# Performance work log

Hardware: AMD Instinct MI355X
Metric: run time of the kernel (lower is better)

Reference implementation:

```python
import jax, jax.numpy as jnp
import numpy as np

B, C, T, L, H = 1024, 32, 9, 24, 8
D = C // H
TOKEN_LEN = 24

def _l2norm(x, eps=1e-12):
    n = jnp.linalg.norm(x, axis=-1, keepdims=True)
    return x / jnp.maximum(n, eps)

def setup_inputs() -> dict:
    key = jax.random.key(0)
    ks = jax.random.split(key, 16)
    def lin_w(k, din, dout):
        return (jax.random.uniform(k, (din, dout), jnp.float32) - 0.5) * (2.0 / np.sqrt(din))
    def lin_b(k, dout, din):
        return (jax.random.uniform(k, (dout,), jnp.float32) - 0.5) * (2.0 / np.sqrt(din))
    inp = {}
    inp['x'] = jax.random.normal(ks[0], (B, C, T, L), jnp.float32)
    inp['Wq'] = lin_w(ks[1], C, C); inp['bq'] = lin_b(ks[2], C, C)
    inp['Wk'] = lin_w(ks[3], C, C); inp['bk'] = lin_b(ks[4], C, C)
    inp['Wv'] = lin_w(ks[5], C, C); inp['bv'] = lin_b(ks[6], C, C)
    inp['Wm'] = lin_w(ks[7], C, C); inp['bm'] = lin_b(ks[8], C, C)
    inp['W_logit'] = jnp.eye(H, dtype=jnp.float32)
    inp['W_ctx'] = jnp.eye(H, dtype=jnp.float32)
    inp['rel_pos_bias'] = jax.random.normal(ks[9], (H, 2 * TOKEN_LEN - 1), jnp.float32) * 0.02
    inp['pre_prompt'] = jax.random.normal(ks[10], (1, C, T, TOKEN_LEN), jnp.float32) * 0.02
    inp['conv_w'] = jax.random.normal(ks[11], (C, C, 3, 3), jnp.float32) / np.sqrt(C * 9)
    inp['conv_b'] = jnp.zeros((C,), jnp.float32)
    inp['bn_gamma'] = jnp.ones((C,), jnp.float32)
    inp['bn_beta'] = jnp.zeros((C,), jnp.float32)
    inp['bn_mean'] = jax.random.normal(ks[12], (C,), jnp.float32) * 0.1
    inp['bn_var'] = jax.random.uniform(ks[13], (C,), jnp.float32) * 0.5 + 0.75
    inp['p_w'] = lin_w(ks[14], TOKEN_LEN, 6).T  # torch Linear(24,6) weight: (6,24)
    inp['p_b'] = lin_b(ks[15], 6, TOKEN_LEN)
    inp['atten_flag'] = 2
    return inp

def reference(x, Wq, bq, Wk, bk, Wv, bv, Wm, bm, W_logit, W_ctx, rel_pos_bias,
              pre_prompt, conv_w, conv_b, bn_gamma, bn_beta, bn_mean, bn_var,
              p_w, p_b, atten_flag):
    b, c, t, l = x.shape
    xp = jnp.transpose(x, (0, 2, 3, 1))  # (b,t,l,c)
    def heads(W, bias):
        y = xp @ W + bias
        return jnp.transpose(y.reshape(b, t, l, H, D), (0, 1, 3, 2, 4))  # (b,t,h,l,d)
    q = _l2norm(heads(Wq, bq))
    k = _l2norm(heads(Wk, bk))
    v = _l2norm(heads(Wv, bv))
    logits = jnp.einsum('bthid,bthjd->bthij', q, k) / np.sqrt(D).astype(np.float32)
    idx = jnp.arange(l)
    rel = jnp.clip(idx[:, None] - idx[None, :] + TOKEN_LEN - 1, 0, 2 * TOKEN_LEN - 2)
    logits = logits + rel_pos_bias[:, rel][None, None]  # bias: (h,l,l)
    logits = jnp.einsum('bthij,hH->btHij', logits, W_logit)
    attn = jax.nn.softmax(logits, axis=-1)
    attn = jnp.einsum('bthij,hH->btHij', attn, W_ctx)
    x_att = jnp.einsum('bthij,bthjd->bthid', attn, v)
    x_att = jnp.transpose(x_att, (0, 1, 3, 2, 4)).reshape(b, t, l, c) @ Wm + bm
    x_att = jnp.transpose(x_att, (0, 3, 1, 2))  # (b,c,t,l)
    pre = jnp.broadcast_to(pre_prompt, (b, c, t, l))
    if atten_flag == 1:
        con = jnp.concatenate([x_att[..., :18], pre[..., 18:]], -1); tar = x_att[..., 18:]
    elif atten_flag == 2:
        con = jnp.concatenate([x_att[..., :12], pre[..., 12:18], x_att[..., 18:]], -1); tar = x_att[..., 12:18]
    elif atten_flag == 3:
        con = jnp.concatenate([x_att[..., :6], pre[..., 6:12], x_att[..., 12:]], -1); tar = x_att[..., 6:12]
    else:
        con = jnp.concatenate([pre[..., :6], x_att[..., 6:]], -1); tar = x_att[..., :6]
    # ConvNormAct(32,32,3,1): Conv2d(3x3, same pad) + BatchNorm2d(eval) + ReLU
    y = jax.lax.conv_general_dilated(con, conv_w, (1, 1), 'SAME',
                                     dimension_numbers=('NCHW', 'OIHW', 'NCHW'))
    y = y + conv_b[None, :, None, None]
    y = (y - bn_mean[None, :, None, None]) * jax.lax.rsqrt(bn_var[None, :, None, None] + 1e-5)
    y = y * bn_gamma[None, :, None, None] + bn_beta[None, :, None, None]
    y = jax.nn.relu(y)
    p = jnp.einsum('bctl,ol->bcto', y, p_w) + p_b  # Linear(token_len, 6) on last dim
    p = tar - p
    if atten_flag == 1:
        out = jnp.concatenate([x_att[..., :18], p], -1)
    elif atten_flag == 2:
        out = jnp.concatenate([x_att[..., :12], p, x_att[..., 18:]], -1)
    elif atten_flag == 3:
        out = jnp.concatenate([x_att[..., :6], p, x_att[..., 12:]], -1)
    else:
        out = jnp.concatenate([p, x_att[..., 6:]], -1)
    return out  # dropout is identity in eval mode
```

## Files before the change

kernel.cpp:

```cpp
#include <hip/hip_runtime.h>
#include <hip/hip_bf16.h>

#define NB   1024
#define NC   32
#define NT   9
#define NL   24
#define CTL  6912
#define TOK  216
#define QSTR 872
#define NTHR 512

typedef _Float16 f16x8 __attribute__((ext_vector_type(8)));
typedef _Float16 f16x4 __attribute__((ext_vector_type(4)));
typedef float    f32x4 __attribute__((ext_vector_type(4)));

#define OFF_BIGA 0
#define SZ_BIGA  41856
#define OFF_BIGB (OFF_BIGA + SZ_BIGA)
#define OFF_WM   (OFF_BIGB + 7680)
#define OFF_BIGC (OFF_WM + 2560)
#define OFF_SPRE (OFF_BIGC + 20480)
#define OFF_REL  (OFF_SPRE + 4320)
#define OFF_WL   (OFF_REL + 1504)
#define OFF_WC   (OFF_WL + 256)
#define OFF_BQKV (OFF_WC + 256)
#define OFF_BM   (OFF_BQKV + 384)
#define OFF_AC   (OFF_BM + 128)
#define OFF_BC   (OFF_AC + 128)
#define OFF_PW   (OFF_BC + 128)
#define OFF_PB   (OFF_PW + 576)
#define OFF_FLG  (OFF_PB + 24)
#define POOL_SZ  80288

static __device__ __forceinline__ float ldf(const void* p, size_t i, bool f32) {
    return f32 ? ((const float*)p)[i]
               : __bfloat162float(((const __hip_bfloat16*)p)[i]);
}
static __device__ __forceinline__ void stf(void* p, size_t i, float v, bool f32) {
    if (f32) ((float*)p)[i] = v;
    else     ((__hip_bfloat16*)p)[i] = __float2bfloat16(v);
}
static __device__ __forceinline__ f32x4 mfma16(f16x8 a, f16x8 b, f32x4 c) {
    return __builtin_amdgcn_mfma_f32_16x16x32_f16(a, b, c, 0, 0, 0);
}

__global__ __launch_bounds__(NTHR, 4) void fused_kernel(
    const void* __restrict__ x,
    const void* __restrict__ Wq, const void* __restrict__ bq,
    const void* __restrict__ Wk, const void* __restrict__ bk,
    const void* __restrict__ Wv, const void* __restrict__ bv,
    const void* __restrict__ Wm, const void* __restrict__ bm,
    const void* __restrict__ Wl, const void* __restrict__ Wc,
    const void* __restrict__ rel, const void* __restrict__ pre,
    const void* __restrict__ cw, const void* __restrict__ cb,
    const void* __restrict__ gmm, const void* __restrict__ bta,
    const void* __restrict__ mean, const void* __restrict__ var,
    const void* __restrict__ p_w, const void* __restrict__ p_b,
    const int* __restrict__ atten_flag,
    void* __restrict__ out)
{
    __shared__ __align__(16) char pool[POOL_SZ];

    const bool f32p = (((const unsigned*)Wl)[0] == 0x3F800000u);
    const int tid  = threadIdx.x;
    const int b    = blockIdx.x;
    const int lane = tid & 63;
    const int wave = tid >> 6;
    const int l15  = lane & 15;
    const int quad = lane >> 4;
    const int grp  = lane & ~7;

    const int flag = atten_flag[0];
    const int s = (flag == 1) ? 18 : (flag == 2) ? 12 : (flag == 3) ? 6 : 0;

    {
        _Float16* xT  = (_Float16*)(pool + OFF_BIGA);
        _Float16* atH = (_Float16*)(pool + OFF_BIGC);
        _Float16* Wqk = (_Float16*)(pool + OFF_BIGB);
        _Float16* WmH = (_Float16*)(pool + OFF_WM);
        _Float16* prH = (_Float16*)(pool + OFF_SPRE);
        float* relF = (float*)(pool + OFF_REL);
        float* wlF  = (float*)(pool + OFF_WL);
        float* wcF  = (float*)(pool + OFF_WC);
        float* bqk  = (float*)(pool + OFF_BQKV);
        float* bmF  = (float*)(pool + OFF_BM);
        float* acF  = (float*)(pool + OFF_AC);
        float* bcF  = (float*)(pool + OFF_BC);
        float* pwF  = (float*)(pool + OFF_PW);
        float* pbF  = (float*)(pool + OFF_PB);

        for (int i = tid; i < CTL; i += NTHR) {
            int c = i / TOK, tok = i % TOK;
            xT[tok*40 + c] = (_Float16)ldf(x, (size_t)b*CTL + i, f32p);
        }
        for (int i = tid; i < 1600; i += NTHR) {
            xT[8640 + i]  = (_Float16)0.f;
            atH[8640 + i] = (_Float16)0.f;
        }
        for (int i = tid; i < 3072; i += NTHR) {
            int mat = i >> 10, r = i & 1023, ci = r >> 5, co = r & 31;
            const void* W = (mat == 0) ? Wq : (mat == 1) ? Wk : Wv;
            Wqk[(mat*32 + co)*40 + ci] = (_Float16)ldf(W, r, f32p);
        }
        for (int i = tid; i < 1024; i += NTHR) {
            int ci = i >> 5, co = i & 31;
            WmH[co*40 + ci] = (_Float16)ldf(Wm, i, f32p);
        }
        for (int i = tid; i < 1728; i += NTHR) {
            int ci = i / 54, r = i % 54, tt = r / 6, o = r % 6;
            prH[(tt*6 + o)*40 + ci] = (_Float16)ldf(pre, (ci*9 + tt)*24 + s + o, f32p);
        }
        for (int i = tid; i < 376; i += NTHR) relF[i] = ldf(rel, i, f32p);
        if (tid < 64)  wlF[tid] = ldf(Wl, tid, f32p);
        if (tid >= 64 && tid < 128) wcF[tid-64] = ldf(Wc, tid-64, f32p);
        if (tid >= 128 && tid < 224) {
            int i = tid - 128; int mat = i >> 5;
            const void* bb = (mat == 0) ? bq : (mat == 1) ? bk : bv;
            bqk[i] = ldf(bb, i & 31, f32p);
        }
        if (tid >= 224 && tid < 256) bmF[tid-224] = ldf(bm, tid-224, f32p);
        if (tid < 32) {
            float rs = rsqrtf(ldf(var, tid, f32p) + 1e-5f);
            float A  = ldf(gmm, tid, f32p) * rs;
            acF[tid] = A;
            bcF[tid] = (ldf(cb, tid, f32p) - ldf(mean, tid, f32p)) * A
                       + ldf(bta, tid, f32p);
        }
        if (tid >= 32 && tid < 176) pwF[tid-32] = ldf(p_w, tid-32, f32p);
        if (tid >= 176 && tid < 182) pbF[tid-176] = ldf(p_b, tid-176, f32p);
    }
    __syncthreads();

    if (tid < 2) {
        const float* M = (const float*)(pool + (tid == 0 ? OFF_WL : OFF_WC));
        int id = 1;
        for (int i = 0; i < 64; i++)
            id &= (M[i] == ((i % 9 == 0) ? 1.f : 0.f));
        ((int*)(pool + OFF_FLG))[tid] = id;
    }

    {
        const _Float16* xT  = (const _Float16*)(pool + OFF_BIGA);
        const _Float16* Wqk = (const _Float16*)(pool + OFF_BIGB);
        f32x4 acc[2][6];
        #pragma unroll
        for (int im = 0; im < 2; im++)
            #pragma unroll
            for (int nt = 0; nt < 6; nt++) acc[im][nt] = 0.f;
        f16x8 bfr[6];
        #pragma unroll
        for (int nt = 0; nt < 6; nt++)
            bfr[nt] = *(const f16x8*)(Wqk + (nt*16 + l15)*40 + quad*8);
        #pragma unroll
        for (int im = 0; im < 2; im++) {
            const int mt = wave + im*8;
            if (mt < 14) {
                f16x8 a = *(const f16x8*)(xT + (mt*16 + l15)*40 + quad*8);
                #pragma unroll
                for (int nt = 0; nt < 6; nt++)
                    acc[im][nt] = mfma16(a, bfr[nt], acc[im][nt]);
            }
        }
        __syncthreads();
        _Float16* qH = (_Float16*)(pool + OFF_BIGA);
        const float* bqk = (const float*)(pool + OFF_BQKV);
        #pragma unroll
        for (int im = 0; im < 2; im++) {
            const int mt = wave + im*8;
            if (mt < 14) {
                #pragma unroll
                for (int nt = 0; nt < 6; nt++) {
                    int co = nt*16 + l15;
                    int mat = co >> 5, hc = co & 31;
                    _Float16* dst = qH + (mat*8 + (hc >> 2))*QSTR + (hc & 3);
                    float bias = bqk[co];
                    #pragma unroll
                    for (int r = 0; r < 4; r++) {
                        int tok = mt*16 + quad*4 + r;
                        if (tok < 216) dst[tok*4] = (_Float16)(acc[im][nt][r] + bias);
                    }
                }
            }
        }
    }
    __syncthreads();

    {
        _Float16* qH = (_Float16*)(pool + OFF_BIGA);
        for (int idx = tid; idx < 3*8*216; idx += NTHR) {
            int plane = idx / 216, tok = idx % 216;
            f16x4* pv = (f16x4*)(qH + plane*QSTR + tok*4);
            f16x4 v = *pv;
            float a0 = v[0], a1 = v[1], a2 = v[2], a3 = v[3];
            float s2 = a0*a0 + a1*a1 + a2*a2 + a3*a3;
            float sc = ((plane < 8) ? 0.5f : 1.0f) / fmaxf(sqrtf(s2), 1e-12f);
            f16x4 nv;
            nv[0] = (_Float16)(a0*sc); nv[1] = (_Float16)(a1*sc);
            nv[2] = (_Float16)(a2*sc); nv[3] = (_Float16)(a3*sc);
            *pv = nv;
        }
    }
    __syncthreads();

    {
        const int idWl = ((int*)(pool + OFF_FLG))[0];
        const int idWc = ((int*)(pool + OFF_FLG))[1];
        const _Float16* qH = (const _Float16*)(pool + OFF_BIGA);
        _Float16* attH = (_Float16*)(pool + OFF_BIGC);
        const float* srel = (const float*)(pool + OFF_REL);
        const float* wlF  = (const float*)(pool + OFF_WL);
        const float* wcF  = (const float*)(pool + OFF_WC);

        for (int idx = tid; idx < 1728; idx += NTHR) {
            int t = idx / 192, r = idx % 192, i = r >> 3, h = r & 7;
            int tb = t * 24;
            f16x4 qv = *(const f16x4*)(qH + h*QSTR + (tb + i)*4);
            float q0 = qv[0], q1 = qv[1], q2 = qv[2], q3 = qv[3];
            const _Float16* kB = qH + (8 + h)*QSTR + tb*4;
            const float* rl = srel + h*47 + i + 23;
            float sc[24];
            #pragma unroll
            for (int j = 0; j < 24; j++) {
                f16x4 kv = *(const f16x4*)(kB + j*4);
                sc[j] = q0*(float)kv[0] + q1*(float)kv[1]
                      + q2*(float)kv[2] + q3*(float)kv[3] + rl[-j];
            }
            if (!idWl) {
                float wl[8], mx[24];
                #pragma unroll
                for (int hh = 0; hh < 8; hh++) wl[hh] = wlF[hh*8 + h];
                #pragma unroll
                for (int j = 0; j < 24; j++) mx[j] = 0.f;
                #pragma unroll
                for (int hh = 0; hh < 8; hh++) {
                    float c = wl[hh];
                    #pragma unroll
                    for (int j = 0; j < 24; j++)
                        mx[j] += c * __shfl(sc[j], grp + hh);
                }
                #pragma unroll
                for (int j = 0; j < 24; j++) sc[j] = mx[j];
            }
            float m = sc[0];
            #pragma unroll
            for (int j = 1; j < 24; j++) m = fmaxf(m, sc[j]);
            float ssum = 0.f;
            #pragma unroll
            for (int j = 0; j < 24; j++) { sc[j] = __expf(sc[j] - m); ssum += sc[j]; }
            float inv = 1.0f / ssum;
            #pragma unroll
            for (int j = 0; j < 24; j++) sc[j] *= inv;

            float wc8[8];
            if (!idWc) {
                #pragma unroll
                for (int hh = 0; hh < 8; hh++) wc8[hh] = wcF[hh*8 + h];
            }
            const _Float16* vB = qH + (16 + h)*QSTR + tb*4;
            float o0 = 0.f, o1 = 0.f, o2 = 0.f, o3 = 0.f;
            #pragma unroll
            for (int j = 0; j < 24; j++) {
                float a2;
                if (idWc) a2 = sc[j];
                else {
                    a2 = 0.f;
                    #pragma unroll
                    for (int hh = 0; hh < 8; hh++)
                        a2 += wc8[hh] * __shfl(sc[j], grp + hh);
                }
                f16x4 vv = *(const f16x4*)(vB + j*4);
                o0 += a2*(float)vv[0]; o1 += a2*(float)vv[1];
                o2 += a2*(float)vv[2]; o3 += a2*(float)vv[3];
            }
            f16x4 ov;
            ov[0] = (_Float16)o0; ov[1] = (_Float16)o1;
            ov[2] = (_Float16)o2; ov[3] = (_Float16)o3;
            *(f16x4*)(attH + (tb + i)*40 + h*4) = ov;
        }
    }
    __syncthreads();

    f32x4 acc4[2][2];
    {
        const _Float16* aH  = (const _Float16*)(pool + OFF_BIGC);
        const _Float16* WmH = (const _Float16*)(pool + OFF_WM);
        #pragma unroll
        for (int im = 0; im < 2; im++) { acc4[im][0] = 0.f; acc4[im][1] = 0.f; }
        f16x8 bf2[2];
        #pragma unroll
        for (int nt = 0; nt < 2; nt++)
            bf2[nt] = *(const f16x8*)(WmH + (nt*16 + l15)*40 + quad*8);
        #pragma unroll
        for (int im = 0; im < 2; im++) {
            const int mt = wave + im*8;
            if (mt < 14) {
                f16x8 a = *(const f16x8*)(aH + (mt*16 + l15)*40 + quad*8);
                acc4[im][0] = mfma16(a, bf2[0], acc4[im][0]);
                acc4[im][1] = mfma16(a, bf2[1], acc4[im][1]);
            }
        }
        _Float16* cwH = (_Float16*)(pool + OFF_BIGA);
        for (int i = tid; i < 9216; i += NTHR) {
            int co = i / 288, rr = i % 288, ci = rr / 9, sh = rr % 9;
            cwH[(sh*32 + co)*40 + ci] = (_Float16)ldf(cw, i, f32p);
        }
    }
    __syncthreads();
    {
        _Float16* sconH = (_Float16*)(pool + OFF_BIGC);
        float* starF = (float*)(pool + OFF_BIGB);
        const float* bmF = (const float*)(pool + OFF_BM);
        #pragma unroll
        for (int im = 0; im < 2; im++) {
            const int mt = wave + im*8;
            if (mt < 14) {
                #pragma unroll
                for (int nt = 0; nt < 2; nt++) {
                    int co = nt*16 + l15;
                    float bias = bmF[co];
                    #pragma unroll
                    for (int r = 0; r < 4; r++) {
                        int tok = mt*16 + quad*4 + r;
                        if (tok < 216) {
                            float v = acc4[im][nt][r] + bias;
                            sconH[tok*40 + co] = (_Float16)v;
                            int t = tok / 24, l = tok % 24, lo = l - s;
                            if (lo >= 0 && lo < 6) starF[(co*9 + t)*6 + lo] = v;
                        }
                    }
                }
            }
        }
    }
    __syncthreads();

    f32x4 accc[2][2];
    {
        const _Float16* sconH = (const _Float16*)(pool + OFF_BIGC);
        const _Float16* prH   = (const _Float16*)(pool + OFF_SPRE);
        const _Float16* cwH   = (const _Float16*)(pool + OFF_BIGA);
        #pragma unroll
        for (int im = 0; im < 2; im++) { accc[im][0] = 0.f; accc[im][1] = 0.f; }
        int tA[2], lA[2], okA[2];
        #pragma unroll
        for (int im = 0; im < 2; im++) {
            const int mt = wave + im*8;
            int tok = mt*16 + l15;
            okA[im] = tok < 216;
            int tc = okA[im] ? tok : 0;
            tA[im] = tc / 24; lA[im] = tc % 24;
        }
        f16x8 zf = 0;
        for (int sh = 0; sh < 9; sh++) {
            int dt = sh/3 - 1, dl = sh%3 - 1;
            f16x8 b0 = *(const f16x8*)(cwH + (sh*32 + l15)*40 + quad*8);
            f16x8 b1 = *(const f16x8*)(cwH + (sh*32 + 16 + l15)*40 + quad*8);
            #pragma unroll
            for (int im = 0; im < 2; im++) {
                const int mt = wave + im*8;
                if (mt < 14) {
                    int tt = tA[im] + dt, ll = lA[im] + dl;
                    bool valid = okA[im] && tt >= 0 && tt < 9 && ll >= 0 && ll < 24;
                    int ttc = valid ? tt : 0, llc = valid ? ll : 0;
                    bool inT = (llc >= s) && (llc < s + 6);
                    const _Float16* ab = inT ? (prH + (ttc*6 + (llc - s))*40)
                                             : (sconH + (ttc*24 + llc)*40);
                    f16x8 a = *(const f16x8*)(ab + quad*8);
                    if (!valid) a = zf;
                    accc[im][0] = mfma16(a, b0, accc[im][0]);
                    accc[im][1] = mfma16(a, b1, accc[im][1]);
                }
            }
        }
    }
    __syncthreads();
    {
        float* yF = (float*)(pool + OFF_BIGA);
        const float* acF = (const float*)(pool + OFF_AC);
        const float* bcF = (const float*)(pool + OFF_BC);
        #pragma unroll
        for (int im = 0; im < 2; im++) {
            const int mt = wave + im*8;
            if (mt < 14) {
                #pragma unroll
                for (int nt = 0; nt < 2; nt++) {
                    int co = nt*16 + l15;
                    float A = acF[co], Bc = bcF[co];
                    #pragma unroll
                    for (int r = 0; r < 4; r++) {
                        int tok = mt*16 + quad*4 + r;
                        if (tok < 216) {
                            int t = tok / 24, l = tok % 24;
                            yF[(co*9 + t)*24 + l] = fmaxf(accc[im][nt][r]*A + Bc, 0.f);
                        }
                    }
                }
            }
        }
    }
    __syncthreads();

    {
        const float* yF  = (const float*)(pool + OFF_BIGA);
        float* starF     = (float*)(pool + OFF_BIGB);
        const float* pwF = (const float*)(pool + OFF_PW);
        const float* pbF = (const float*)(pool + OFF_PB);
        for (int idx = tid; idx < NC*NT*6; idx += NTHR) {
            int co = idx / 54, r = idx % 54, t = r / 6, o = r % 6;
            const float* yr = yF + (co*9 + t)*24;
            float p = pbF[o];
            #pragma unroll
            for (int l = 0; l < 24; l++) p += yr[l] * pwF[o*24 + l];
            starF[idx] = starF[(co*9 + t)*6 + o] - p;
        }
    }
    __syncthreads();

    {
        const _Float16* sconH = (const _Float16*)(pool + OFF_BIGC);
        const float* resF = (const float*)(pool + OFF_BIGB);
        if (f32p) {
            float* of = (float*)out + (size_t)b*CTL;
            for (int i4 = tid; i4 < CTL/4; i4 += NTHR) {
                int i = i4 * 4;
                int co = i / TOK, tok0 = i % TOK;
                float4 v;
                float* vp = (float*)&v;
                #pragma unroll
                for (int k = 0; k < 4; k++) {
                    int tok = tok0 + k;
                    int t = tok / 24, l = tok % 24, lo = l - s;
                    vp[k] = (lo >= 0 && lo < 6) ? resF[(co*9 + t)*6 + lo]
                                                : (float)sconH[tok*40 + co];
                }
                *(float4*)(of + i) = v;
            }
        } else {
            for (int i = tid; i < CTL; i += NTHR) {
                int co = i / TOK, tok = i % TOK;
                int t = tok / 24, l = tok % 24, lo = l - s;
                float v = (lo >= 0 && lo < 6) ? resF[(co*9 + t)*6 + lo]
                                              : (float)sconH[tok*40 + co];
                stf(out, (size_t)b*CTL + i, v, f32p);
            }
        }
    }
}

extern "C" void kernel_launch(void* const* d_in, const int* in_sizes, int n_in,
                              void* d_out, int out_size, void* d_ws, size_t ws_size,
                              hipStream_t stream) {
    (void)d_ws; (void)ws_size; (void)in_sizes; (void)n_in; (void)out_size;
    fused_kernel<<<NB, NTHR, 0, stream>>>(
        d_in[0], d_in[1], d_in[2], d_in[3], d_in[4], d_in[5], d_in[6],
        d_in[7], d_in[8], d_in[9], d_in[10], d_in[11], d_in[12], d_in[13],
        d_in[14], d_in[15], d_in[16], d_in[17], d_in[18], d_in[19], d_in[20],
        (const int*)d_in[21], d_out);
}
```

Baseline: 204.4 us.

## Double block size, vectorize loads, use fdot2 and transposed V layout in attention

Raises threads per block from 512 to 1024 so each wave handles a single MFMA row tile, and removes the per-wave im loops. It also vectorizes the fp32 global loads of x, weights and conv weights with float4, and stores V transposed per dimension so the PV product can use packed fp16 dot2 instructions. The softmax drops the max subtraction, which is safe only because q and k are L2-normalised and the logits stay small, and the code switches to fast rsq/rcp intrinsics. The risks are lower occupancy headroom from the larger block, register pressure, and fp16 rounding of the attention probabilities.

```diff
diff --git a/kernel.cpp b/kernel.cpp
--- a/kernel.cpp
+++ b/kernel.cpp
@@ -7,15 +7,17 @@
 #define NL   24
 #define CTL  6912
 #define TOK  216
-#define QSTR 872
-#define NTHR 512
+#define QSTR 880
+#define VROW 220
+#define NTHR 1024
 
 typedef _Float16 f16x8 __attribute__((ext_vector_type(8)));
 typedef _Float16 f16x4 __attribute__((ext_vector_type(4)));
+typedef _Float16 f16x2 __attribute__((ext_vector_type(2)));
 typedef float    f32x4 __attribute__((ext_vector_type(4)));
 
 #define OFF_BIGA 0
-#define SZ_BIGA  41856
+#define SZ_BIGA  42240
 #define OFF_BIGB (OFF_BIGA + SZ_BIGA)
 #define OFF_WM   (OFF_BIGB + 7680)
 #define OFF_BIGC (OFF_WM + 2560)
@@ -30,7 +32,7 @@
 #define OFF_PW   (OFF_BC + 128)
 #define OFF_PB   (OFF_PW + 576)
 #define OFF_FLG  (OFF_PB + 24)
-#define POOL_SZ  80288
+#define POOL_SZ  80672
 
 static __device__ __forceinline__ float ldf(const void* p, size_t i, bool f32) {
     return f32 ? ((const float*)p)[i]
@@ -43,8 +45,36 @@
 static __device__ __forceinline__ f32x4 mfma16(f16x8 a, f16x8 b, f32x4 c) {
     return __builtin_amdgcn_mfma_f32_16x16x32_f16(a, b, c, 0, 0, 0);
 }
-
-__global__ __launch_bounds__(NTHR, 4) void fused_kernel(
+static __device__ __forceinline__ float fdot2(f16x2 a, f16x2 b, float c) {
+#if __has_builtin(__builtin_amdgcn_fdot2)
+    return __builtin_amdgcn_fdot2(a, b, c, false);
+#else
+    return c + (float)a[0]*(float)b[0] + (float)a[1]*(float)b[1];
+#endif
+}
+static __device__ __forceinline__ f16x2 pack2(float lo, float hi) {
+#if __has_builtin(__builtin_amdgcn_cvt_pkrtz)
+    return __builtin_bit_cast(f16x2, __builtin_amdgcn_cvt_pkrtz(lo, hi));
+#else
+    f16x2 r; r[0] = (_Float16)lo; r[1] = (_Float16)hi; return r;
+#endif
+}
+static __device__ __forceinline__ float rsq_f(float x) {
+#if __has_builtin(__builtin_amdgcn_rsqf)
+    return __builtin_amdgcn_rsqf(x);
+#else
+    return rsqrtf(x);
+#endif
+}
+static __device__ __forceinline__ float rcp_f(float x) {
+#if __has_builtin(__builtin_amdgcn_rcpf)
+    return __builtin_amdgcn_rcpf(x);
+#else
+    return 1.0f / x;
+#endif
+}
+
+__global__ __launch_bounds__(NTHR, 8) void fused_kernel(
     const void* __restrict__ x,
     const void* __restrict__ Wq, const void* __restrict__ bq,
     const void* __restrict__ Wk, const void* __restrict__ bk,
@@ -89,22 +119,56 @@
         float* pwF  = (float*)(pool + OFF_PW);
         float* pbF  = (float*)(pool + OFF_PB);
 
-        for (int i = tid; i < CTL; i += NTHR) {
-            int c = i / TOK, tok = i % TOK;
-            xT[tok*40 + c] = (_Float16)ldf(x, (size_t)b*CTL + i, f32p);
+        if (f32p) {
+            const float4* xf4 = (const float4*)((const float*)x + (size_t)b*CTL);
+            for (int i4 = tid; i4 < CTL/4; i4 += NTHR) {
+                float4 v = xf4[i4];
+                int i = i4 << 2;
+                int c = i / TOK, tok = i % TOK;
+                _Float16* dst = xT + tok*40 + c;
+                dst[0]   = (_Float16)v.x;
+                dst[40]  = (_Float16)v.y;
+                dst[80]  = (_Float16)v.z;
+                dst[120] = (_Float16)v.w;
+            }
+            for (int i4 = tid; i4 < 768; i4 += NTHR) {
+                int mat = i4 >> 8, r4 = i4 & 255;
+                int ci = r4 >> 3, co = (r4 & 7) << 2;
+                const void* W = (mat == 0) ? Wq : (mat == 1) ? Wk : Wv;
+                float4 v = ((const float4*)W)[r4];
+                _Float16* dst = Wqk + (mat*32 + co)*40 + ci;
+                dst[0]   = (_Float16)v.x;
+                dst[40]  = (_Float16)v.y;
+                dst[80]  = (_Float16)v.z;
+                dst[120] = (_Float16)v.w;
+            }
+            for (int i4 = tid; i4 < 256; i4 += NTHR) {
+                int ci = i4 >> 3, co = (i4 & 7) << 2;
+                float4 v = ((const float4*)Wm)[i4];
+                _Float16* dst = WmH + co*40 + ci;
+                dst[0]   = (_Float16)v.x;
+                dst[40]  = (_Float16)v.y;
+                dst[80]  = (_Float16)v.z;
+                dst[120] = (_Float16)v.w;
+            }
+        } else {
+            for (int i = tid; i < CTL; i += NTHR) {
+                int c = i / TOK, tok = i % TOK;
+                xT[tok*40 + c] = (_Float16)ldf(x, (size_t)b*CTL + i, f32p);
+            }
+            for (int i = tid; i < 3072; i += NTHR) {
+                int mat = i >> 10, r = i & 1023, ci = r >> 5, co = r & 31;
+                const void* W = (mat == 0) ? Wq : (mat == 1) ? Wk : Wv;
+                Wqk[(mat*32 + co)*40 + ci] = (_Float16)ldf(W, r, f32p);
+            }
+            for (int i = tid; i < 1024; i += NTHR) {
+                int ci = i >> 5, co = i & 31;
+                WmH[co*40 + ci] = (_Float16)ldf(Wm, i, f32p);
+            }
         }
         for (int i = tid; i < 1600; i += NTHR) {
             xT[8640 + i]  = (_Float16)0.f;
             atH[8640 + i] = (_Float16)0.f;
-        }
-        for (int i = tid; i < 3072; i += NTHR) {
-            int mat = i >> 10, r = i & 1023, ci = r >> 5, co = r & 31;
-            const void* W = (mat == 0) ? Wq : (mat == 1) ? Wk : Wv;
-            Wqk[(mat*32 + co)*40 + ci] = (_Float16)ldf(W, r, f32p);
-        }
-        for (int i = tid; i < 1024; i += NTHR) {
-            int ci = i >> 5, co = i & 31;
-            WmH[co*40 + ci] = (_Float16)ldf(Wm, i, f32p);
         }
         for (int i = tid; i < 1728; i += NTHR) {
             int ci = i / 54, r = i % 54, tt = r / 6, o = r % 6;
@@ -142,43 +206,43 @@
     {
         const _Float16* xT  = (const _Float16*)(pool + OFF_BIGA);
         const _Float16* Wqk = (const _Float16*)(pool + OFF_BIGB);
-        f32x4 acc[2][6];
+        f32x4 acc[6];
         #pragma unroll
-        for (int im = 0; im < 2; im++)
-            #pragma unroll
-            for (int nt = 0; nt < 6; nt++) acc[im][nt] = 0.f;
+        for (int nt = 0; nt < 6; nt++) acc[nt] = 0.f;
         f16x8 bfr[6];
         #pragma unroll
         for (int nt = 0; nt < 6; nt++)
             bfr[nt] = *(const f16x8*)(Wqk + (nt*16 + l15)*40 + quad*8);
-        #pragma unroll
-        for (int im = 0; im < 2; im++) {
-            const int mt = wave + im*8;
-            if (mt < 14) {
-                f16x8 a = *(const f16x8*)(xT + (mt*16 + l15)*40 + quad*8);
-                #pragma unroll
-                for (int nt = 0; nt < 6; nt++)
-                    acc[im][nt] = mfma16(a, bfr[nt], acc[im][nt]);
-            }
+        const int mt = wave;
+        if (mt < 14) {
+            f16x8 a = *(const f16x8*)(xT + (mt*16 + l15)*40 + quad*8);
+            #pragma unroll
+            for (int nt = 0; nt < 6; nt++)
+                acc[nt] = mfma16(a, bfr[nt], acc[nt]);
         }
         __syncthreads();
         _Float16* qH = (_Float16*)(pool + OFF_BIGA);
         const float* bqk = (const float*)(pool + OFF_BQKV);
-        #pragma unroll
-        for (int im = 0; im < 2; im++) {
-            const int mt = wave + im*8;
-            if (mt < 14) {
-                #pragma unroll
-                for (int nt = 0; nt < 6; nt++) {
-                    int co = nt*16 + l15;
-                    int mat = co >> 5, hc = co & 31;
+        if (mt < 14) {
+            #pragma unroll
+            for (int nt = 0; nt < 6; nt++) {
+                int co = nt*16 + l15;
+                int mat = co >> 5, hc = co & 31;
+                float bias = bqk[co];
+                if (mat < 2) {
                     _Float16* dst = qH + (mat*8 + (hc >> 2))*QSTR + (hc & 3);
-                    float bias = bqk[co];
                     #pragma unroll
                     for (int r = 0; r < 4; r++) {
                         int tok = mt*16 + quad*4 + r;
-                        if (tok < 216) dst[tok*4] = (_Float16)(acc[im][nt][r] + bias);
+                        if (tok < 216) dst[tok*4] = (_Float16)(acc[nt][r] + bias);
                     }
+                } else {
+                    _Float16* dst = qH + (16 + (hc >> 2))*QSTR + (hc & 3)*VROW;
+                    #pragma unroll
+                    for (int r = 0; r < 4; r++) {
+                        int tok = mt*16 + quad*4 + r;
+                        if (tok < 216) dst[tok] = (_Float16)(acc[nt][r] + bias);
+                    }
                 }
             }
         }
@@ -187,17 +251,28 @@
 
     {
         _Float16* qH = (_Float16*)(pool + OFF_BIGA);
-        for (int idx = tid; idx < 3*8*216; idx += NTHR) {
+        for (int idx = tid; idx < 16*216; idx += NTHR) {
             int plane = idx / 216, tok = idx % 216;
             f16x4* pv = (f16x4*)(qH + plane*QSTR + tok*4);
             f16x4 v = *pv;
             float a0 = v[0], a1 = v[1], a2 = v[2], a3 = v[3];
             float s2 = a0*a0 + a1*a1 + a2*a2 + a3*a3;
-            float sc = ((plane < 8) ? 0.5f : 1.0f) / fmaxf(sqrtf(s2), 1e-12f);
+            float sc = ((plane < 8) ? 0.5f : 1.0f) * rsq_f(fmaxf(s2, 1e-24f));
             f16x4 nv;
             nv[0] = (_Float16)(a0*sc); nv[1] = (_Float16)(a1*sc);
             nv[2] = (_Float16)(a2*sc); nv[3] = (_Float16)(a3*sc);
             *pv = nv;
+        }
+        for (int idx = tid; idx < 8*216; idx += NTHR) {
+            int h = idx / 216, tok = idx % 216;
+            _Float16* vp = qH + (16 + h)*QSTR + tok;
+            float a0 = vp[0], a1 = vp[VROW], a2 = vp[2*VROW], a3 = vp[3*VROW];
+            float s2 = a0*a0 + a1*a1 + a2*a2 + a3*a3;
+            float sc = rsq_f(fmaxf(s2, 1e-24f));
+            vp[0]      = (_Float16)(a0*sc);
+            vp[VROW]   = (_Float16)(a1*sc);
+            vp[2*VROW] = (_Float16)(a2*sc);
+            vp[3*VROW] = (_Float16)(a3*sc);
         }
     }
     __syncthreads();
@@ -214,16 +289,15 @@
         for (int idx = tid; idx < 1728; idx += NTHR) {
             int t = idx / 192, r = idx % 192, i = r >> 3, h = r & 7;
             int tb = t * 24;
-            f16x4 qv = *(const f16x4*)(qH + h*QSTR + (tb + i)*4);
-            float q0 = qv[0], q1 = qv[1], q2 = qv[2], q3 = qv[3];
+            const f16x2* qp = (const f16x2*)(qH + h*QSTR + (tb + i)*4);
+            f16x2 q01 = qp[0], q23 = qp[1];
             const _Float16* kB = qH + (8 + h)*QSTR + tb*4;
             const float* rl = srel + h*47 + i + 23;
             float sc[24];
             #pragma unroll
             for (int j = 0; j < 24; j++) {
-                f16x4 kv = *(const f16x4*)(kB + j*4);
-                sc[j] = q0*(float)kv[0] + q1*(float)kv[1]
-                      + q2*(float)kv[2] + q3*(float)kv[3] + rl[-j];
+                const f16x2* kp = (const f16x2*)(kB + j*4);
+                sc[j] = fdot2(q01, kp[0], fdot2(q23, kp[1], rl[-j]));
             }
             if (!idWl) {
                 float wl[8], mx[24];
@@ -241,68 +315,89 @@
                 #pragma unroll
                 for (int j = 0; j < 24; j++) sc[j] = mx[j];
             }
-            float m = sc[0];
-            #pragma unroll
-            for (int j = 1; j < 24; j++) m = fmaxf(m, sc[j]);
             float ssum = 0.f;
             #pragma unroll
-            for (int j = 0; j < 24; j++) { sc[j] = __expf(sc[j] - m); ssum += sc[j]; }
-            float inv = 1.0f / ssum;
+            for (int j = 0; j < 24; j++) { sc[j] = __expf(sc[j]); ssum += sc[j]; }
+            float inv = rcp_f(ssum);
             #pragma unroll
             for (int j = 0; j < 24; j++) sc[j] *= inv;
-
-            float wc8[8];
             if (!idWc) {
+                float wc8[8], mx[24];
                 #pragma unroll
                 for (int hh = 0; hh < 8; hh++) wc8[hh] = wcF[hh*8 + h];
-            }
-            const _Float16* vB = qH + (16 + h)*QSTR + tb*4;
-            float o0 = 0.f, o1 = 0.f, o2 = 0.f, o3 = 0.f;
-            #pragma unroll
-            for (int j = 0; j < 24; j++) {
-                float a2;
-                if (idWc) a2 = sc[j];
-                else {
-                    a2 = 0.f;
+                #pragma unroll
+                for (int j = 0; j < 24; j++) mx[j] = 0.f;
+                #pragma unroll
+                for (int hh = 0; hh < 8; hh++) {
+                    float c = wc8[hh];
                     #pragma unroll
-                    for (int hh = 0; hh < 8; hh++)
-                        a2 += wc8[hh] * __shfl(sc[j], grp + hh);
-                }
-                f16x4 vv = *(const f16x4*)(vB + j*4);
-                o0 += a2*(float)vv[0]; o1 += a2*(float)vv[1];
-                o2 += a2*(float)vv[2]; o3 += a2*(float)vv[3];
+                    for (int j = 0; j < 24; j++)
+                        mx[j] += c * __shfl(sc[j], grp + hh);
+                }
+                #pragma unroll
+                for (int j = 0; j < 24; j++) sc[j] = mx[j];
+            }
+            f16x2 pa[12];
+            #pragma unroll
+            for (int jp = 0; jp < 12; jp++)
+                pa[jp] = pack2(sc[2*jp], sc[2*jp + 1]);
+            const _Float16* vbase = qH + (16 + h)*QSTR + tb;
+            float o[4];
+            #pragma unroll
+            for (int d = 0; d < 4; d++) {
+                const f16x4* vr = (const f16x4*)(vbase + d*VROW);
+                float od = 0.f;
+                #pragma unroll
+                for (int jj = 0; jj < 6; jj++) {
+                    f16x4 vv = vr[jj];
+                    f16x2 vlo = __builtin_shufflevector(vv, vv, 0, 1);
+                    f16x2 vhi = __builtin_shufflevector(vv, vv, 2, 3);
+                    od = fdot2(pa[2*jj],     vlo, od);
+                    od = fdot2(pa[2*jj + 1], vhi, od);
+                }
+                o[d] = od;
             }
             f16x4 ov;
-            ov[0] = (_Float16)o0; ov[1] = (_Float16)o1;
-            ov[2] = (_Float16)o2; ov[3] = (_Float16)o3;
+            ov[0] = (_Float16)o[0]; ov[1] = (_Float16)o[1];
+            ov[2] = (_Float16)o[2]; ov[3] = (_Float16)o[3];
             *(f16x4*)(attH + (tb + i)*40 + h*4) = ov;
         }
     }
     __syncthreads();
 
-    f32x4 acc4[2][2];
+    f32x4 acc4[2];
     {
         const _Float16* aH  = (const _Float16*)(pool + OFF_BIGC);
         const _Float16* WmH = (const _Float16*)(pool + OFF_WM);
-        #pragma unroll
-        for (int im = 0; im < 2; im++) { acc4[im][0] = 0.f; acc4[im][1] = 0.f; }
+        acc4[0] = 0.f; acc4[1] = 0.f;
         f16x8 bf2[2];
         #pragma unroll
         for (int nt = 0; nt < 2; nt++)
             bf2[nt] = *(const f16x8*)(WmH + (nt*16 + l15)*40 + quad*8);
-        #pragma unroll
-        for (int im = 0; im < 2; im++) {
-            const int mt = wave + im*8;
-            if (mt < 14) {
-                f16x8 a = *(const f16x8*)(aH + (mt*16 + l15)*40 + quad*8);
-                acc4[im][0] = mfma16(a, bf2[0], acc4[im][0]);
-                acc4[im][1] = mfma16(a, bf2[1], acc4[im][1]);
-            }
+        const int mt = wave;
+        if (mt < 14) {
+            f16x8 a = *(const f16x8*)(aH + (mt*16 + l15)*40 + quad*8);
+            acc4[0] = mfma16(a, bf2[0], acc4[0]);
+            acc4[1] = mfma16(a, bf2[1], acc4[1]);
         }
         _Float16* cwH = (_Float16*)(pool + OFF_BIGA);
-        for (int i = tid; i < 9216; i += NTHR) {
-            int co = i / 288, rr = i % 288, ci = rr / 9, sh = rr % 9;
-            cwH[(sh*32 + co)*40 + ci] = (_Float16)ldf(cw, i, f32p);
+        if (f32p) {
+            for (int i4 = tid; i4 < 2304; i4 += NTHR) {
+                int i = i4 << 2;
+                int co = i / 288, rr = i % 288;
+                float4 v = ((const float4*)cw)[i4];
+                float vv[4] = {v.x, v.y, v.z, v.w};
+                #pragma unroll
+                for (int k = 0; k < 4; k++) {
+                    int ci = (rr + k) / 9, sh = (rr + k) % 9;
+                    cwH[(sh*32 + co)*40 + ci] = (_Float16)vv[k];
+                }
+            }
+        } else {
+            for (int i = tid; i < 9216; i += NTHR) {
+                int co = i / 288, rr = i % 288, ci = rr / 9, sh = rr % 9;
+                cwH[(sh*32 + co)*40 + ci] = (_Float16)ldf(cw, i, f32p);
+            }
         }
     }
     __syncthreads();
@@ -310,23 +405,20 @@
         _Float16* sconH = (_Float16*)(pool + OFF_BIGC);
         float* starF = (float*)(pool + OFF_BIGB);
         const float* bmF = (const float*)(pool + OFF_BM);
-        #pragma unroll
-        for (int im = 0; im < 2; im++) {
-            const int mt = wave + im*8;
-            if (mt < 14) {
-                #pragma unroll
-                for (int nt = 0; nt < 2; nt++) {
-                    int co = nt*16 + l15;
-                    float bias = bmF[co];
-                    #pragma unroll
-                    for (int r = 0; r < 4; r++) {
-                        int tok = mt*16 + quad*4 + r;
-                        if (tok < 216) {
-                            float v = acc4[im][nt][r] + bias;
-                            sconH[tok*40 + co] = (_Float16)v;
-                            int t = tok / 24, l = tok % 24, lo = l - s;
-                            if (lo >= 0 && lo < 6) starF[(co*9 + t)*6 + lo] = v;
-                        }
+        const int mt = wave;
+        if (mt < 14) {
+            #pragma unroll
+            for (int nt = 0; nt < 2; nt++) {
+                int co = nt*16 + l15;
+                float bias = bmF[co];
+                #pragma unroll
+                for (int r = 0; r < 4; r++) {
+                    int tok = mt*16 + quad*4 + r;
+                    if (tok < 216) {
+                        float v = acc4[nt][r] + bias;
+                        sconH[tok*40 + co] = (_Float16)v;
+                        int t = tok / 24, l = tok % 24, lo = l - s;
+                        if (lo >= 0 && lo < 6) starF[(co*9 + t)*6 + lo] = v;
                     }
                 }
             }
@@ -334,42 +426,33 @@
     }
     __syncthreads();
 
-    f32x4 accc[2][2];
+    f32x4 accc[2];
     {
         const _Float16* sconH = (const _Float16*)(pool + OFF_BIGC);
         const _Float16* prH   = (const _Float16*)(pool + OFF_SPRE);
         const _Float16* cwH   = (const _Float16*)(pool + OFF_BIGA);
-        #pragma unroll
-        for (int im = 0; im < 2; im++) { accc[im][0] = 0.f; accc[im][1] = 0.f; }
-        int tA[2], lA[2], okA[2];
-        #pragma unroll
-        for (int im = 0; im < 2; im++) {
-            const int mt = wave + im*8;
-            int tok = mt*16 + l15;
-            okA[im] = tok < 216;
-            int tc = okA[im] ? tok : 0;
-            tA[im] = tc / 24; lA[im] = tc % 24;
-        }
+        accc[0] = 0.f; accc[1] = 0.f;
+        const int mt = wave;
+        int tok0 = mt*16 + l15;
+        int ok = tok0 < 216;
+        int tc = ok ? tok0 : 0;
+        int tA = tc / 24, lA = tc % 24;
         f16x8 zf = 0;
         for (int sh = 0; sh < 9; sh++) {
             int dt = sh/3 - 1, dl = sh%3 - 1;
             f16x8 b0 = *(const f16x8*)(cwH + (sh*32 + l15)*40 + quad*8);
             f16x8 b1 = *(const f16x8*)(cwH + (sh*32 + 16 + l15)*40 + quad*8);
-            #pragma unroll
-            for (int im = 0; im < 2; im++) {
-                const int mt = wave + im*8;
-                if (mt < 14) {
-                    int tt = tA[im] + dt, ll = lA[im] + dl;
-                    bool valid = okA[im] && tt >= 0 && tt < 9 && ll >= 0 && ll < 24;
-                    int ttc = valid ? tt : 0, llc = valid ? ll : 0;
-                    bool inT = (llc >= s) && (llc < s + 6);
-                    const _Float16* ab = inT ? (prH + (ttc*6 + (llc - s))*40)
-                                             : (sconH + (ttc*24 + llc)*40);
-                    f16x8 a = *(const f16x8*)(ab + quad*8);
-                    if (!valid) a = zf;
-                    accc[im][0] = mfma16(a, b0, accc[im][0]);
-                    accc[im][1] = mfma16(a, b1, accc[im][1]);
-                }
+            if (mt < 14) {
+                int tt = tA + dt, ll = lA + dl;
+                bool valid = ok && tt >= 0 && tt < 9 && ll >= 0 && ll < 24;
+                int ttc = valid ? tt : 0, llc = valid ? ll : 0;
+                bool inT = (llc >= s) && (llc < s + 6);
+                const _Float16* ab = inT ? (prH + (ttc*6 + (llc - s))*40)
+                                         : (sconH + (ttc*24 + llc)*40);
+                f16x8 a = *(const f16x8*)(ab + quad*8);
+                if (!valid) a = zf;
+                accc[0] = mfma16(a, b0, accc[0]);
+                accc[1] = mfma16(a, b1, accc[1]);
             }
         }
     }
@@ -378,21 +461,18 @@
         float* yF = (float*)(pool + OFF_BIGA);
         const float* acF = (const float*)(pool + OFF_AC);
         const float* bcF = (const float*)(pool + OFF_BC);
-        #pragma unroll
-        for (int im = 0; im < 2; im++) {
-            const int mt = wave + im*8;
-            if (mt < 14) {
-                #pragma unroll
-                for (int nt = 0; nt < 2; nt++) {
-                    int co = nt*16 + l15;
-                    float A = acF[co], Bc = bcF[co];
-                    #pragma unroll
-                    for (int r = 0; r < 4; r++) {
-                        int tok = mt*16 + quad*4 + r;
-                        if (tok < 216) {
-                            int t = tok / 24, l = tok % 24;
-                            yF[(co*9 + t)*24 + l] = fmaxf(accc[im][nt][r]*A + Bc, 0.f);
-                        }
+        const int mt = wave;
+        if (mt < 14) {
+            #pragma unroll
+            for (int nt = 0; nt < 2; nt++) {
+                int co = nt*16 + l15;
+                float A = acF[co], Bc = bcF[co];
+                #pragma unroll
+                for (int r = 0; r < 4; r++) {
+                    int tok = mt*16 + quad*4 + r;
+                    if (tok < 216) {
+                        int t = tok / 24, l = tok % 24;
+                        yF[(co*9 + t)*24 + l] = fmaxf(accc[nt][r]*A + Bc, 0.f);
                     }
                 }
             }
@@ -407,11 +487,13 @@
         const float* pbF = (const float*)(pool + OFF_PB);
         for (int idx = tid; idx < NC*NT*6; idx += NTHR) {
             int co = idx / 54, r = idx % 54, t = r / 6, o = r % 6;
-            const float* yr = yF + (co*9 + t)*24;
-            float p = pbF[o];
-            #pragma unroll
-            for (int l = 0; l < 24; l++) p += yr[l] * pwF[o*24 + l];
-            starF[idx] = starF[(co*9 + t)*6 + o] - p;
+            const f32x4* yr = (const f32x4*)(yF + (co*9 + t)*24);
+            const f32x4* pw = (const f32x4*)(pwF + o*24);
+            f32x4 s4 = yr[0] * pw[0];
+            #pragma unroll
+            for (int l4 = 1; l4 < 6; l4++) s4 += yr[l4] * pw[l4];
+            float p = pbF[o] + s4[0] + s4[1] + s4[2] + s4[3];
+            starF[idx] = starF[idx] - p;
         }
     }
     __syncthreads();
```

Result: faster. 175.8 us (-14.0%).
